# Performance work log

Hardware: AMD Instinct MI355X
Metric: run time of the kernel (lower is better)

Reference implementation:

```python
import jax, jax.numpy as jnp
import numpy as np

EPS = 1e-6
NEG = -1e9
RES_RATIO = 1.0  # res_ratio init arg
MAKE_SYM = True


def _ln(x, g, b):
    m = jnp.mean(x, axis=-1, keepdims=True)
    v = jnp.mean((x - m) ** 2, axis=-1, keepdims=True)
    return (x - m) * jax.lax.rsqrt(v + EPS) * g + b


def _sim(q, k, W1q, W1k, b1, W2, b2):
    # NN(concat([q,k])) with first dense split into query/key halves:
    # relu(q@W1q + k@W1k + b1) @ W2 + b2  -> avoids materializing the 2d concat.
    qa = q @ W1q  # [b,n,sq,h]
    kb = k @ W1k  # [b,n,sk,h]
    h1 = jax.nn.relu(qa[:, :, :, None, :] + kb[:, :, None, :, :] + b1)  # [b,n,sq,sk,h]
    s = jnp.einsum('bnqkh,h->bnqk', h1, W2[:, 0]) + b2[0]
    if MAKE_SYM:
        qb = q @ W1k
        ka = k @ W1q
        h2 = jax.nn.relu(ka[:, :, None, :, :] + qb[:, :, :, None, :] + b1)
        s = s + jnp.einsum('bnqkh,h->bnqk', h2, W2[:, 0]) + b2[0]
    return s


def _attention(v, k, q, mask, Ww, bw, Wd, bd, W1q, W1k, b1, W2, b2):
    q = q @ Ww + bw
    k = k @ Ww + bw
    v = v @ Ww + bw
    logits = _sim(q, k, W1q, W1k, b1, W2, b2)
    if mask is not None:
        logits = logits + mask * NEG
    attn = jax.nn.softmax(logits, axis=-1)
    out = jnp.einsum('bnqk,bnkd->bnqd', attn, v)
    return out @ Wd + bd, attn


def setup_inputs() -> dict:
    key = jax.random.key(0)
    B, N, S, D, DFF, H = 4, 1, 256, 128, 512, 128
    ks = jax.random.split(key, 16)
    s = 0.02
    inp = {
        'x': jax.random.normal(ks[0], (B, N, S, D), jnp.float32),
        'enc_output': jax.random.normal(ks[1], (B, N, S, D), jnp.float32),
        'com_mask': jnp.zeros((B, N, S, S), jnp.float32),
        'dec_mask': jnp.zeros((B, N, S, S), jnp.float32),
        # shared pairwise-score MLP NN: Dense(H, relu) -> Dense(1)
        'W1q': jax.random.normal(ks[2], (D, H), jnp.float32) * s,
        'W1k': jax.random.normal(ks[3], (D, H), jnp.float32) * s,
        'b1': jnp.zeros((H,), jnp.float32),
        'W2': jax.random.normal(ks[4], (H, 1), jnp.float32) * s,
        'b2': jnp.zeros((1,), jnp.float32),
        # mha1 projections
        'Ww1': jax.random.normal(ks[5], (D, D), jnp.float32) * s,
        'bw1': jnp.zeros((D,), jnp.float32),
        'Wd1': jax.random.normal(ks[6], (D, D), jnp.float32) * s,
        'bd1': jnp.zeros((D,), jnp.float32),
        # mha2 projections
        'Ww2': jax.random.normal(ks[7], (D, D), jnp.float32) * s,
        'bw2': jnp.zeros((D,), jnp.float32),
        'Wd2': jax.random.normal(ks[8], (D, D), jnp.float32) * s,
        'bd2': jnp.zeros((D,), jnp.float32),
        # ffn
        'Wf1': jax.random.normal(ks[9], (D, DFF), jnp.float32) * s,
        'bf1': jnp.zeros((DFF,), jnp.float32),
        'Wf2': jax.random.normal(ks[10], (DFF, D), jnp.float32) * s,
        'bf2': jnp.zeros((D,), jnp.float32),
        # layernorms
        'ln1_g': jnp.ones((D,), jnp.float32), 'ln1_b': jnp.zeros((D,), jnp.float32),
        'ln2_g': jnp.ones((D,), jnp.float32), 'ln2_b': jnp.zeros((D,), jnp.float32),
        'ln3_g': jnp.ones((D,), jnp.float32), 'ln3_b': jnp.zeros((D,), jnp.float32),
    }
    return inp


def reference(x, enc_output, com_mask, dec_mask,
              W1q, W1k, b1, W2, b2,
              Ww1, bw1, Wd1, bd1,
              Ww2, bw2, Wd2, bd2,
              Wf1, bf1, Wf2, bf2,
              ln1_g, ln1_b, ln2_g, ln2_b, ln3_g, ln3_b):
    r = RES_RATIO
    # self-attention block (dropout inactive, eval mode)
    attn1, aw1 = _attention(x, x, x, com_mask, Ww1, bw1, Wd1, bd1, W1q, W1k, b1, W2, b2)
    out1 = _ln((2 - r) * attn1 + r * x, ln1_g, ln1_b)
    # cross-attention block
    attn2, aw2 = _attention(enc_output, enc_output, out1, dec_mask, Ww2, bw2, Wd2, bd2, W1q, W1k, b1, W2, b2)
    out2 = _ln((2 - r) * attn2 + r * out1, ln2_g, ln2_b)
    # ffn
    ffn = jax.nn.relu(out2 @ Wf1 + bf1) @ Wf2 + bf2
    out3 = _ln((2 - r) * ffn + r * out2, ln3_g, ln3_b)
    return out3
```

## Files before the change

### kernel.cpp

```cpp
#include <hip/hip_runtime.h>
#include <math.h>


#define LN_EPS 1e-6f
#define NEGV  (-1e9f)

constexpr int B = 4, S = 256, D = 128, H = 128, DFF = 512;
constexpr int R = B * S;
constexpr int LDW = H + 4;

struct P {
    const float *x, *enc, *com_mask, *dec_mask;
    const float *W1q, *W1k, *b1, *W2;
    const float *Ww1, *bw1, *Wd1, *bd1;
    const float *Ww2, *bw2, *Wd2, *bd2;
    const float *Wf1, *bf1, *Wf2, *bf2;
    const float *ln1g, *ln1b, *ln2g, *ln2b, *ln3g, *ln3b;
    float *out;
    float *xw, *qa, *kb, *kv2w, *kb2, *ka2, *qa2, *qb2;
    float *sbuf, *sbuf2, *out1;
};

__global__ __launch_bounds__(512) void proj3_kernel(P p)
{
    const int g = blockIdx.y, tid = threadIdx.x;
    const int r0 = blockIdx.x * 8;
    __shared__ __align__(16) float Ash[8 * 128];
    __shared__ __align__(16) float Pw[8 * 128];
    __shared__ __align__(16) float Pp[2 * 8 * 128];

    const float* A    = g ? p.enc  : p.x;
    const float* Wp   = g ? p.Ww2  : p.Ww1;
    const float* bp   = g ? p.bw2  : p.bw1;
    float*       o_w  = g ? p.kv2w : p.xw;
    const float* Wsec = g ? p.W1k  : p.W1q;
    const float* bsec = g ? nullptr: p.b1;
    float*       o_s  = g ? p.kb2  : p.qa;
    const float* Wthr = g ? p.W1q  : p.W1k;
    float*       o_t  = g ? p.ka2  : p.kb;

    if (tid < 256)
        ((float4*)Ash)[tid] = ((const float4*)(A + (size_t)r0 * 128))[tid];
    __syncthreads();

    {
        const int kh = tid >> 8, unit = tid & 255, lr = unit >> 5, c4 = unit & 31;
        const float4* W4 = (const float4*)Wp;
        float4 acc = (kh == 0) ? ((const float4*)bp)[c4] : make_float4(0.f, 0.f, 0.f, 0.f);
        const int k0 = kh * 64;
        #pragma unroll 8
        for (int k = 0; k < 64; ++k) {
            const float a = Ash[lr * 128 + k0 + k];
            const float4 w = W4[(k0 + k) * 32 + c4];
            acc.x = fmaf(a, w.x, acc.x); acc.y = fmaf(a, w.y, acc.y);
            acc.z = fmaf(a, w.z, acc.z); acc.w = fmaf(a, w.w, acc.w);
        }
        ((float4*)Pp)[kh * 256 + unit] = acc;
    }
    __syncthreads();
    if (tid < 256) {
        const int lr = tid >> 5, c4 = tid & 31;
        const float4 a = ((const float4*)Pp)[tid];
        const float4 bq = ((const float4*)Pp)[256 + tid];
        const float4 w = make_float4(a.x + bq.x, a.y + bq.y, a.z + bq.z, a.w + bq.w);
        ((float4*)Pw)[tid] = w;
        ((float4*)o_w)[(size_t)(r0 + lr) * 32 + c4] = w;
    }
    __syncthreads();

    {
        const int which = tid >> 8, unit = tid & 255, lr = unit >> 5, c4 = unit & 31;
        const float* W = which ? Wthr : Wsec;
        const float* bb = which ? nullptr : bsec;
        float* o = which ? o_t : o_s;
        const float4* W4 = (const float4*)W;
        float4 acc = bb ? ((const float4*)bb)[c4] : make_float4(0.f, 0.f, 0.f, 0.f);
        #pragma unroll 8
        for (int k = 0; k < 128; ++k) {
            const float a = Pw[lr * 128 + k];
            const float4 w = W4[k * 32 + c4];
            acc.x = fmaf(a, w.x, acc.x); acc.y = fmaf(a, w.y, acc.y);
            acc.z = fmaf(a, w.z, acc.z); acc.w = fmaf(a, w.w, acc.w);
        }
        ((float4*)o)[(size_t)(r0 + lr) * 32 + c4] = acc;
    }
}

#define PW_STEP_N(AP0, AP1, BP0, BP1, A00, A01, A10, A11)                      \
    {                                                                          \
        const float4 w  = *(const float4*)(W2s + h);                           \
        const float4 a0 = *(const float4*)((AP0) + h);                         \
        const float4 a1 = *(const float4*)((AP1) + h);                         \
        const float4 b0 = *(const float4*)((BP0) + h);                         \
        const float4 b1 = *(const float4*)((BP1) + h);                         \
        A00 = fmaf(fmaxf(a0.x+b0.x,0.f),w.x,A00); A00 = fmaf(fmaxf(a0.y+b0.y,0.f),w.y,A00); \
        A00 = fmaf(fmaxf(a0.z+b0.z,0.f),w.z,A00); A00 = fmaf(fmaxf(a0.w+b0.w,0.f),w.w,A00); \
        A01 = fmaf(fmaxf(a0.x+b1.x,0.f),w.x,A01); A01 = fmaf(fmaxf(a0.y+b1.y,0.f),w.y,A01); \
        A01 = fmaf(fmaxf(a0.z+b1.z,0.f),w.z,A01); A01 = fmaf(fmaxf(a0.w+b1.w,0.f),w.w,A01); \
        A10 = fmaf(fmaxf(a1.x+b0.x,0.f),w.x,A10); A10 = fmaf(fmaxf(a1.y+b0.y,0.f),w.y,A10); \
        A10 = fmaf(fmaxf(a1.z+b0.z,0.f),w.z,A10); A10 = fmaf(fmaxf(a1.w+b0.w,0.f),w.w,A10); \
        A11 = fmaf(fmaxf(a1.x+b1.x,0.f),w.x,A11); A11 = fmaf(fmaxf(a1.y+b1.y,0.f),w.y,A11); \
        A11 = fmaf(fmaxf(a1.z+b1.z,0.f),w.z,A11); A11 = fmaf(fmaxf(a1.w+b1.w,0.f),w.w,A11); \
    }

__global__ __launch_bounds__(512) void pairwise_self_kernel(P p)
{
    __shared__ __align__(16) float As[32 * LDW];
    __shared__ __align__(16) float Bs[32 * LDW];
    __shared__ __align__(16) float W2s[H];
    __shared__ __align__(16) float Pp[256 * 4];
    const int b = blockIdx.z, q0 = blockIdx.y * 32, k0 = blockIdx.x * 32;
    const int tid = threadIdx.x, bS = b * S;
    for (int i = tid; i < 32 * (H / 4); i += 512) {
        const int r = i >> 5, c4 = i & 31;
        ((float4*)(As + r * LDW))[c4] = ((const float4*)(p.qa + (size_t)(bS + q0 + r) * H))[c4];
        ((float4*)(Bs + r * LDW))[c4] = ((const float4*)(p.kb + (size_t)(bS + k0 + r) * H))[c4];
    }
    if (tid < H / 4) ((float4*)W2s)[tid] = ((const float4*)p.W2)[tid];
    __syncthreads();
    const int hh = tid >> 8, unit = tid & 255;
    const int tx = unit & 15, ty = unit >> 4;
    const float* A0 = As + (2 * ty) * LDW; const float* A1 = A0 + LDW;
    const float* B0 = Bs + (2 * tx) * LDW; const float* B1 = B0 + LDW;
    float acc00 = 0.f, acc01 = 0.f, acc10 = 0.f, acc11 = 0.f;
    const int hbase = hh * 64;
    #pragma unroll 4
    for (int hi = 0; hi < 64; hi += 4) {
        const int h = hbase + hi;
        PW_STEP_N(A0, A1, B0, B1, acc00, acc01, acc10, acc11);
    }
    if (hh) ((float4*)Pp)[unit] = make_float4(acc00, acc01, acc10, acc11);
    __syncthreads();
    if (!hh) {
        const float4 o = ((const float4*)Pp)[unit];
        const size_t base = (size_t)(bS + q0 + 2 * ty) * S + (k0 + 2 * tx);
        *(float2*)(p.sbuf + base)     = make_float2(acc00 + o.x, acc01 + o.y);
        *(float2*)(p.sbuf + base + S) = make_float2(acc10 + o.z, acc11 + o.w);
    }
}

__global__ __launch_bounds__(512) void pairwise_cross2_kernel(P p)
{
    __shared__ __align__(16) float As1[32 * LDW];
    __shared__ __align__(16) float Bs1[32 * LDW];
    __shared__ __align__(16) float As2[32 * LDW];
    __shared__ __align__(16) float Bs2[32 * LDW];
    __shared__ __align__(16) float W2s[H];
    __shared__ __align__(16) float Pp8[256 * 8];
    const int b = blockIdx.z, q0 = blockIdx.y * 32, k0 = blockIdx.x * 32;
    const int tid = threadIdx.x, bS = b * S;

    for (int i = tid; i < 32 * (H / 4); i += 512) {
        const int r = i >> 5, c4 = i & 31;
        ((float4*)(As1 + r * LDW))[c4] = ((const float4*)(p.qa2 + (size_t)(bS + q0 + r) * H))[c4];
        ((float4*)(Bs1 + r * LDW))[c4] = ((const float4*)(p.kb2 + (size_t)(bS + k0 + r) * H))[c4];
        ((float4*)(As2 + r * LDW))[c4] = ((const float4*)(p.qb2 + (size_t)(bS + q0 + r) * H))[c4];
        ((float4*)(Bs2 + r * LDW))[c4] = ((const float4*)(p.ka2 + (size_t)(bS + k0 + r) * H))[c4];
    }
    if (tid < H / 4) ((float4*)W2s)[tid] = ((const float4*)p.W2)[tid];
    __syncthreads();

    const int hh = tid >> 8, unit = tid & 255;
    const int tx = unit & 15, ty = unit >> 4;
    const float* A0 = As1 + (2 * ty) * LDW; const float* A1 = A0 + LDW;
    const float* B0 = Bs1 + (2 * tx) * LDW; const float* B1 = B0 + LDW;
    const float* C0 = As2 + (2 * ty) * LDW; const float* C1 = C0 + LDW;
    const float* D0 = Bs2 + (2 * tx) * LDW; const float* D1 = D0 + LDW;
    float a00 = 0.f, a01 = 0.f, a10 = 0.f, a11 = 0.f;
    float b00 = 0.f, b01 = 0.f, b10 = 0.f, b11 = 0.f;
    const int hbase = hh * 64;
    #pragma unroll 4
    for (int hi = 0; hi < 64; hi += 4) {
        const int h = hbase + hi;
        PW_STEP_N(A0, A1, B0, B1, a00, a01, a10, a11);
        PW_STEP_N(C0, C1, D0, D1, b00, b01, b10, b11);
    }
    if (hh) {
        ((float4*)Pp8)[unit * 2]     = make_float4(a00, a01, a10, a11);
        ((float4*)Pp8)[unit * 2 + 1] = make_float4(b00, b01, b10, b11);
    }
    __syncthreads();
    if (!hh) {
        const float4 o1 = ((const float4*)Pp8)[unit * 2];
        const float4 o2 = ((const float4*)Pp8)[unit * 2 + 1];
        const size_t base = (size_t)(bS + q0 + 2 * ty) * S + (k0 + 2 * tx);
        *(float2*)(p.sbuf2 + base)     = make_float2(a00 + b00 + o1.x + o2.x, a01 + b01 + o1.y + o2.y);
        *(float2*)(p.sbuf2 + base + S) = make_float2(a10 + b10 + o1.z + o2.z, a11 + b11 + o1.w + o2.w);
    }
}

template<bool SYM, bool QPROJ, bool FFN>
__global__ __launch_bounds__(512) void attn_tail_kernel(P p)
{
    __shared__ __align__(16) float smem[FFN ? 16896 : 6144];
    float* rowS = smem;
    float* s8   = smem + 512;
    float* avp  = smem + 1536;
    float* aoS  = smem + 3584;
    float* pp   = smem + 4096;

    const float* Sin  = SYM ? p.sbuf : p.sbuf2;
    const float* mask = SYM ? p.com_mask : p.dec_mask;
    const float* V    = SYM ? p.xw : p.kv2w;
    const float* Wd   = SYM ? p.Wd1 : p.Wd2;
    const float* bd   = SYM ? p.bd1 : p.bd2;
    const float* res  = SYM ? p.x : p.out1;
    const float* lg   = SYM ? p.ln1g : p.ln2g;
    const float* lb   = SYM ? p.ln1b : p.ln2b;

    const int tid = threadIdx.x;
    const int r0 = blockIdx.x * 4, b = r0 >> 8, bS = b * S;

    for (int i = tid; i < 4 * 256; i += 512) {
        const int r = i >> 8, k = i & 255;
        const int row = r0 + r, q = row & 255;
        float l = Sin[(size_t)row * S + k];
        if (SYM) l += Sin[(size_t)(bS + k) * S + q];
        l += mask[(size_t)row * S + k] * NEGV;
        s8[i] = l;
    }
    __syncthreads();

    {
        const int g = tid >> 6, c = tid & 63;
        if (g < 4) {
            float* rowp = s8 + g * 256;
            float m = -INFINITY;
            #pragma unroll
            for (int k = c; k < 256; k += 64) m = fmaxf(m, rowp[k]);
            for (int o = 32; o; o >>= 1) m = fmaxf(m, __shfl_xor(m, o, 64));
            float s = 0.f;
            #pragma unroll
            for (int k = c; k < 256; k += 64) { const float e = __expf(rowp[k] - m); rowp[k] = e; s += e; }
            for (int o = 32; o; o >>= 1) s += __shfl_xor(s, o, 64);
            const float rinv = 1.f / s;
            #pragma unroll
            for (int k = c; k < 256; k += 64) rowp[k] *= rinv;
        }
    }
    __syncthreads();

    {
        const int r = tid >> 7, t = tid & 127, kq = t >> 5, c4 = t & 31;
        const float4* V4 = (const float4*)(V + (size_t)bS * D);
        const float* sp = s8 + r * 256 + kq * 64;
        float4 acc = make_float4(0.f, 0.f, 0.f, 0.f);
        #pragma unroll 8
        for (int k = 0; k < 64; ++k) {
            const float a = sp[k];
            const float4 v = V4[(kq * 64 + k) * 32 + c4];
            acc.x = fmaf(a, v.x, acc.x); acc.y = fmaf(a, v.y, acc.y);
            acc.z = fmaf(a, v.z, acc.z); acc.w = fmaf(a, v.w, acc.w);
        }
        ((float4*)avp)[(r * 4 + kq) * 32 + c4] = acc;
    }
    __syncthreads();
    if (tid < 128) {
        const int r = tid >> 5, c4 = tid & 31;
        float4 s0 = ((const float4*)avp)[(r * 4 + 0) * 32 + c4];
        const float4 s1 = ((const float4*)avp)[(r * 4 + 1) * 32 + c4];
        const float4 s2 = ((const float4*)avp)[(r * 4 + 2) * 32 + c4];
        const float4 s3 = ((const float4*)avp)[(r * 4 + 3) * 32 + c4];
        s0.x += s1.x + s2.x + s3.x; s0.y += s1.y + s2.y + s3.y;
        s0.z += s1.z + s2.z + s3.z; s0.w += s1.w + s2.w + s3.w;
        ((float4*)aoS)[r * 32 + c4] = s0;
    }
    __syncthreads();

    {
        const int kq = tid >> 7, unit = tid & 127, r = unit >> 5, c4 = unit & 31;
        const float4* W4 = (const float4*)Wd;
        const float* ap = aoS + r * 128 + kq * 32;
        float4 acc = make_float4(0.f, 0.f, 0.f, 0.f);
        #pragma unroll 8
        for (int k = 0; k < 32; ++k) {
            const float a = ap[k];
            const float4 w = W4[(kq * 32 + k) * 32 + c4];
            acc.x = fmaf(a, w.x, acc.x); acc.y = fmaf(a, w.y, acc.y);
            acc.z = fmaf(a, w.z, acc.z); acc.w = fmaf(a, w.w, acc.w);
        }
        ((float4*)pp)[kq * 128 + unit] = acc;
    }
    __syncthreads();

    if (tid < 128) {
        const int r = tid >> 5, c4 = tid & 31;
        const float4 p0 = ((const float4*)pp)[tid];
        const float4 p1 = ((const float4*)pp)[128 + tid];
        const float4 p2 = ((const float4*)pp)[256 + tid];
        const float4 p3 = ((const float4*)pp)[384 + tid];
        const float4 bv0 = ((const float4*)bd)[c4];
        const float4 r4 = ((const float4*)(res + (size_t)(r0 + r) * 128))[c4];
        const float x0 = p0.x + p1.x + p2.x + p3.x + bv0.x + r4.x;
        const float x1 = p0.y + p1.y + p2.y + p3.y + bv0.y + r4.y;
        const float x2 = p0.z + p1.z + p2.z + p3.z + bv0.z + r4.z;
        const float x3 = p0.w + p1.w + p2.w + p3.w + bv0.w + r4.w;
        float s  = x0 + x1 + x2 + x3;
        float s2 = x0 * x0 + x1 * x1 + x2 * x2 + x3 * x3;
        for (int o = 16; o; o >>= 1) { s += __shfl_xor(s, o, 32); s2 += __shfl_xor(s2, o, 32); }
        const float m = s * (1.f / 128), var = s2 * (1.f / 128) - m * m;
        const float rs = rsqrtf(var + LN_EPS);
        const float4 gv = ((const float4*)lg)[c4], bv = ((const float4*)lb)[c4];
        float4 o4;
        o4.x = (x0 - m) * rs * gv.x + bv.x; o4.y = (x1 - m) * rs * gv.y + bv.y;
        o4.z = (x2 - m) * rs * gv.z + bv.z; o4.w = (x3 - m) * rs * gv.w + bv.w;
        ((float4*)rowS)[r * 32 + c4] = o4;
        if (SYM) ((float4*)p.out1)[(size_t)(r0 + r) * 32 + c4] = o4;
    }
    __syncthreads();

    if (QPROJ) {
        float* qpp  = smem + 512;
        float* q2wS = smem + 2560;
        float* qp2  = smem + 1536;
        {
            const int kq = tid >> 7, unit = tid & 127, r = unit >> 5, c4 = unit & 31;
            const float4* W4 = (const float4*)p.Ww2;
            const float* ap = rowS + r * 128 + kq * 32;
            float4 acc = make_float4(0.f, 0.f, 0.f, 0.f);
            #pragma unroll 8
            for (int k = 0; k < 32; ++k) {
                const float a = ap[k];
                const float4 w = W4[(kq * 32 + k) * 32 + c4];
                acc.x = fmaf(a, w.x, acc.x); acc.y = fmaf(a, w.y, acc.y);
                acc.z = fmaf(a, w.z, acc.z); acc.w = fmaf(a, w.w, acc.w);
            }
            ((float4*)qpp)[kq * 128 + unit] = acc;
        }
        __syncthreads();
        if (tid < 128) {
            const int c4 = tid & 31;
            const float4 p0 = ((const float4*)qpp)[tid];
            const float4 p1 = ((const float4*)qpp)[128 + tid];
            const float4 p2 = ((const float4*)qpp)[256 + tid];
            const float4 p3 = ((const float4*)qpp)[384 + tid];
            const float4 bw = ((const float4*)p.bw2)[c4];
            ((float4*)q2wS)[tid] = make_float4(p0.x + p1.x + p2.x + p3.x + bw.x,
                                               p0.y + p1.y + p2.y + p3.y + bw.y,
                                               p0.z + p1.z + p2.z + p3.z + bw.z,
                                               p0.w + p1.w + p2.w + p3.w + bw.w);
        }
        __syncthreads();
        {
            const int which = tid >> 8, sub = tid & 255;
            const int kh = sub >> 7, unit2 = sub & 127;
            const float4* W4 = (const float4*)(which ? p.W1k : p.W1q);
            const int r = unit2 >> 5, c4 = unit2 & 31;
            const float* ap = q2wS + r * 128 + kh * 64;
            float4 acc = make_float4(0.f, 0.f, 0.f, 0.f);
            #pragma unroll 8
            for (int k = 0; k < 64; ++k) {
                const float a = ap[k];
                const float4 w = W4[(kh * 64 + k) * 32 + c4];
                acc.x = fmaf(a, w.x, acc.x); acc.y = fmaf(a, w.y, acc.y);
                acc.z = fmaf(a, w.z, acc.z); acc.w = fmaf(a, w.w, acc.w);
            }
            ((float4*)qp2)[(which * 2 + kh) * 128 + unit2] = acc;
        }
        __syncthreads();
        if (tid < 256) {
            const int which = tid >> 7, unit2 = tid & 127;
            const int r = unit2 >> 5, c4 = unit2 & 31;
            const float4 p0 = ((const float4*)qp2)[(which * 2 + 0) * 128 + unit2];
            const float4 p1 = ((const float4*)qp2)[(which * 2 + 1) * 128 + unit2];
            const float4 b1v = ((const float4*)p.b1)[c4];
            float* oq = which ? p.qb2 : p.qa2;
            ((float4*)oq)[(size_t)(r0 + r) * 32 + c4] =
                make_float4(p0.x + p1.x + b1v.x, p0.y + p1.y + b1v.y,
                            p0.z + p1.z + b1v.z, p0.w + p1.w + b1v.w);
        }
    }

    if (FFN) {
        float* hidP = smem + 512;
        float* part = smem + 8704;
        {
            const int c = tid & 127, kh = tid >> 7;
            const float4* Wf1_4 = (const float4*)p.Wf1;
            float4 a0 = make_float4(0.f,0.f,0.f,0.f), a1 = a0, a2 = a0, a3 = a0;
            const int kbase = kh * 32;
            #pragma unroll 8
            for (int k = 0; k < 32; ++k) {
                const int kk = kbase + k;
                const float4 w = Wf1_4[kk * 128 + c];
                const float s0 = rowS[kk],       s1 = rowS[128 + kk];
                const float s2 = rowS[256 + kk], s3 = rowS[384 + kk];
                a0.x=fmaf(s0,w.x,a0.x); a0.y=fmaf(s0,w.y,a0.y); a0.z=fmaf(s0,w.z,a0.z); a0.w=fmaf(s0,w.w,a0.w);
                a1.x=fmaf(s1,w.x,a1.x); a1.y=fmaf(s1,w.y,a1.y); a1.z=fmaf(s1,w.z,a1.z); a1.w=fmaf(s1,w.w,a1.w);
                a2.x=fmaf(s2,w.x,a2.x); a2.y=fmaf(s2,w.y,a2.y); a2.z=fmaf(s2,w.z,a2.z); a2.w=fmaf(s2,w.w,a2.w);
                a3.x=fmaf(s3,w.x,a3.x); a3.y=fmaf(s3,w.y,a3.y); a3.z=fmaf(s3,w.z,a3.z); a3.w=fmaf(s3,w.w,a3.w);
            }
            float4* h4 = (float4*)hidP;
            const int base = kh * 512;
            h4[base + 0*128 + c] = a0; h4[base + 1*128 + c] = a1;
            h4[base + 2*128 + c] = a2; h4[base + 3*128 + c] = a3;
        }
        __syncthreads();
        for (int i = tid; i < 2048; i += 512) {
            hidP[i] = fmaxf(hidP[i] + hidP[2048 + i] + hidP[4096 + i] + hidP[6144 + i]
                            + p.bf1[i & 511], 0.f);
        }
        __syncthreads();
        {
            const int c4f = tid & 31, kg = tid >> 5;
            const float4* Wf2_4 = (const float4*)p.Wf2;
            float4 a0 = make_float4(0.f,0.f,0.f,0.f), a1 = a0, a2 = a0, a3 = a0;
            const int kbase = kg * 32;
            const float* h0 = hidP + 0 * 512 + kbase;
            const float* h1 = hidP + 1 * 512 + kbase;
            const float* h2 = hidP + 2 * 512 + kbase;
            const float* h3 = hidP + 3 * 512 + kbase;
            #pragma unroll 8
            for (int k = 0; k < 32; ++k) {
                const float4 w = Wf2_4[(kbase + k) * 32 + c4f];
                const float s0 = h0[k], s1 = h1[k], s2 = h2[k], s3 = h3[k];
                a0.x=fmaf(s0,w.x,a0.x); a0.y=fmaf(s0,w.y,a0.y); a0.z=fmaf(s0,w.z,a0.z); a0.w=fmaf(s0,w.w,a0.w);
                a1.x=fmaf(s1,w.x,a1.x); a1.y=fmaf(s1,w.y,a1.y); a1.z=fmaf(s1,w.z,a1.z); a1.w=fmaf(s1,w.w,a1.w);
                a2.x=fmaf(s2,w.x,a2.x); a2.y=fmaf(s2,w.y,a2.y); a2.z=fmaf(s2,w.z,a2.z); a2.w=fmaf(s2,w.w,a2.w);
                a3.x=fmaf(s3,w.x,a3.x); a3.y=fmaf(s3,w.y,a3.y); a3.z=fmaf(s3,w.z,a3.z); a3.w=fmaf(s3,w.w,a3.w);
            }
            float4* p4 = (float4*)part;
            p4[kg * 128 + 0 * 32 + c4f] = a0; p4[kg * 128 + 1 * 32 + c4f] = a1;
            p4[kg * 128 + 2 * 32 + c4f] = a2; p4[kg * 128 + 3 * 32 + c4f] = a3;
        }
        __syncthreads();
        if (tid < 128) {
            const int r = tid >> 5, c4 = tid & 31;
            const float4* p4 = (const float4*)part;
            float4 sum = ((const float4*)p.bf2)[c4];
            #pragma unroll
            for (int kg = 0; kg < 16; ++kg) {
                const float4 v = p4[kg * 128 + r * 32 + c4];
                sum.x += v.x; sum.y += v.y; sum.z += v.z; sum.w += v.w;
            }
            const float4 r4 = ((const float4*)rowS)[r * 32 + c4];
            const float x0 = sum.x + r4.x, x1 = sum.y + r4.y;
            const float x2 = sum.z + r4.z, x3 = sum.w + r4.w;
            float s  = x0 + x1 + x2 + x3;
            float s2 = x0 * x0 + x1 * x1 + x2 * x2 + x3 * x3;
            for (int o = 16; o; o >>= 1) { s += __shfl_xor(s, o, 32); s2 += __shfl_xor(s2, o, 32); }
            const float m = s * (1.f / 128), var = s2 * (1.f / 128) - m * m;
            const float rs = rsqrtf(var + LN_EPS);
            const float4 gv = ((const float4*)p.ln3g)[c4], bv = ((const float4*)p.ln3b)[c4];
            float4 o4;
            o4.x = (x0 - m) * rs * gv.x + bv.x; o4.y = (x1 - m) * rs * gv.y + bv.y;
            o4.z = (x2 - m) * rs * gv.z + bv.z; o4.w = (x3 - m) * rs * gv.w + bv.w;
            ((float4*)p.out)[(size_t)(r0 + r) * 32 + c4] = o4;
        }
    }
}

extern "C" void kernel_launch(void* const* d_in, const int* in_sizes, int n_in,
                              void* d_out, int out_size, void* d_ws, size_t ws_size,
                              hipStream_t stream) {
    (void)in_sizes; (void)n_in; (void)out_size; (void)ws_size;
    P p;
    p.x        = (const float*)d_in[0];
    p.enc      = (const float*)d_in[1];
    p.com_mask = (const float*)d_in[2];
    p.dec_mask = (const float*)d_in[3];
    p.W1q = (const float*)d_in[4];
    p.W1k = (const float*)d_in[5];
    p.b1  = (const float*)d_in[6];
    p.W2  = (const float*)d_in[7];
    p.Ww1 = (const float*)d_in[9];
    p.bw1 = (const float*)d_in[10];
    p.Wd1 = (const float*)d_in[11];
    p.bd1 = (const float*)d_in[12];
    p.Ww2 = (const float*)d_in[13];
    p.bw2 = (const float*)d_in[14];
    p.Wd2 = (const float*)d_in[15];
    p.bd2 = (const float*)d_in[16];
    p.Wf1 = (const float*)d_in[17];
    p.bf1 = (const float*)d_in[18];
    p.Wf2 = (const float*)d_in[19];
    p.bf2 = (const float*)d_in[20];
    p.ln1g = (const float*)d_in[21];
    p.ln1b = (const float*)d_in[22];
    p.ln2g = (const float*)d_in[23];
    p.ln2b = (const float*)d_in[24];
    p.ln3g = (const float*)d_in[25];
    p.ln3b = (const float*)d_in[26];
    p.out  = (float*)d_out;

    float* ws = (float*)d_ws;
    const size_t RD  = (size_t)R * D;
    const size_t SSz = (size_t)B * S * S;
    p.xw    = ws;
    p.qa    = p.xw    + RD;
    p.kb    = p.qa    + RD;
    p.kv2w  = p.kb    + RD;
    p.kb2   = p.kv2w  + RD;
    p.ka2   = p.kb2   + RD;
    p.qa2   = p.ka2   + RD;
    p.qb2   = p.qa2   + RD;
    p.sbuf  = p.qb2   + RD;
    p.sbuf2 = p.sbuf  + SSz;
    p.out1  = p.sbuf2 + SSz;

    proj3_kernel<<<dim3(R / 8, 2), 512, 0, stream>>>(p);
    pairwise_self_kernel<<<dim3(8, 8, 4), 512, 0, stream>>>(p);
    attn_tail_kernel<true, true, false><<<R / 4, 512, 0, stream>>>(p);
    pairwise_cross2_kernel<<<dim3(8, 8, 4), 512, 0, stream>>>(p);
    attn_tail_kernel<false, false, true><<<R / 4, 512, 0, stream>>>(p);
}
```

Before: 172.0 us.

## Fuse pairwise score MLP into attention tail kernels, drop score buffers

Folds the pairwise relu-MLP score computation into each attention tail block. Each block of 4 query rows streams all 256 keys through shared memory in 64-key tiles and reduces across 8 lanes with shuffles. Symmetrization is done directly with both terms for the self block, so the S×S score buffers and two kernel launches go away. The trade-off is that each of the 256 blocks recomputes over all keys with only 4 query rows of reuse, which adds key-side global and LDS traffic per block.

```diff
diff --git a/kernel.cpp b/kernel.cpp
--- a/kernel.cpp
+++ b/kernel.cpp
@@ -7,7 +7,7 @@
 
 constexpr int B = 4, S = 256, D = 128, H = 128, DFF = 512;
 constexpr int R = B * S;
-constexpr int LDW = H + 4;
+constexpr int SP = 132;
 
 struct P {
     const float *x, *enc, *com_mask, *dec_mask;
@@ -17,8 +17,7 @@
     const float *Wf1, *bf1, *Wf2, *bf2;
     const float *ln1g, *ln1b, *ln2g, *ln2b, *ln3g, *ln3b;
     float *out;
-    float *xw, *qa, *kb, *kv2w, *kb2, *ka2, *qa2, *qb2;
-    float *sbuf, *sbuf2, *out1;
+    float *xw, *qa, *kb, *kv2w, *kb2, *ka2, *qa2, *qb2, *out1;
 };
 
 __global__ __launch_bounds__(512) void proj3_kernel(P p)
@@ -86,138 +85,105 @@
     }
 }
 
-#define PW_STEP_N(AP0, AP1, BP0, BP1, A00, A01, A10, A11)                      \
-    {                                                                          \
-        const float4 w  = *(const float4*)(W2s + h);                           \
-        const float4 a0 = *(const float4*)((AP0) + h);                         \
-        const float4 a1 = *(const float4*)((AP1) + h);                         \
-        const float4 b0 = *(const float4*)((BP0) + h);                         \
-        const float4 b1 = *(const float4*)((BP1) + h);                         \
-        A00 = fmaf(fmaxf(a0.x+b0.x,0.f),w.x,A00); A00 = fmaf(fmaxf(a0.y+b0.y,0.f),w.y,A00); \
-        A00 = fmaf(fmaxf(a0.z+b0.z,0.f),w.z,A00); A00 = fmaf(fmaxf(a0.w+b0.w,0.f),w.w,A00); \
-        A01 = fmaf(fmaxf(a0.x+b1.x,0.f),w.x,A01); A01 = fmaf(fmaxf(a0.y+b1.y,0.f),w.y,A01); \
-        A01 = fmaf(fmaxf(a0.z+b1.z,0.f),w.z,A01); A01 = fmaf(fmaxf(a0.w+b1.w,0.f),w.w,A01); \
-        A10 = fmaf(fmaxf(a1.x+b0.x,0.f),w.x,A10); A10 = fmaf(fmaxf(a1.y+b0.y,0.f),w.y,A10); \
-        A10 = fmaf(fmaxf(a1.z+b0.z,0.f),w.z,A10); A10 = fmaf(fmaxf(a1.w+b0.w,0.f),w.w,A10); \
-        A11 = fmaf(fmaxf(a1.x+b1.x,0.f),w.x,A11); A11 = fmaf(fmaxf(a1.y+b1.y,0.f),w.y,A11); \
-        A11 = fmaf(fmaxf(a1.z+b1.z,0.f),w.z,A11); A11 = fmaf(fmaxf(a1.w+b1.w,0.f),w.w,A11); \
-    }
-
-__global__ __launch_bounds__(512) void pairwise_self_kernel(P p)
+#define SC8(ACC, O1, X1, O2, X2)                                               \
+    ACC = fmaf(fmaxf((O1).x + (X1).x, 0.f), w.x, ACC);                         \
+    ACC = fmaf(fmaxf((O1).y + (X1).y, 0.f), w.y, ACC);                         \
+    ACC = fmaf(fmaxf((O1).z + (X1).z, 0.f), w.z, ACC);                         \
+    ACC = fmaf(fmaxf((O1).w + (X1).w, 0.f), w.w, ACC);                         \
+    ACC = fmaf(fmaxf((O2).x + (X2).x, 0.f), w.x, ACC);                         \
+    ACC = fmaf(fmaxf((O2).y + (X2).y, 0.f), w.y, ACC);                         \
+    ACC = fmaf(fmaxf((O2).z + (X2).z, 0.f), w.z, ACC);                         \
+    ACC = fmaf(fmaxf((O2).w + (X2).w, 0.f), w.w, ACC);
+
+template<bool FIRST>
+__global__ __launch_bounds__(512) void fused_attn_kernel(P p)
 {
-    __shared__ __align__(16) float As[32 * LDW];
-    __shared__ __align__(16) float Bs[32 * LDW];
-    __shared__ __align__(16) float W2s[H];
-    __shared__ __align__(16) float Pp[256 * 4];
-    const int b = blockIdx.z, q0 = blockIdx.y * 32, k0 = blockIdx.x * 32;
-    const int tid = threadIdx.x, bS = b * S;
-    for (int i = tid; i < 32 * (H / 4); i += 512) {
-        const int r = i >> 5, c4 = i & 31;
-        ((float4*)(As + r * LDW))[c4] = ((const float4*)(p.qa + (size_t)(bS + q0 + r) * H))[c4];
-        ((float4*)(Bs + r * LDW))[c4] = ((const float4*)(p.kb + (size_t)(bS + k0 + r) * H))[c4];
-    }
-    if (tid < H / 4) ((float4*)W2s)[tid] = ((const float4*)p.W2)[tid];
-    __syncthreads();
-    const int hh = tid >> 8, unit = tid & 255;
-    const int tx = unit & 15, ty = unit >> 4;
-    const float* A0 = As + (2 * ty) * LDW; const float* A1 = A0 + LDW;
-    const float* B0 = Bs + (2 * tx) * LDW; const float* B1 = B0 + LDW;
-    float acc00 = 0.f, acc01 = 0.f, acc10 = 0.f, acc11 = 0.f;
-    const int hbase = hh * 64;
-    #pragma unroll 4
-    for (int hi = 0; hi < 64; hi += 4) {
-        const int h = hbase + hi;
-        PW_STEP_N(A0, A1, B0, B1, acc00, acc01, acc10, acc11);
-    }
-    if (hh) ((float4*)Pp)[unit] = make_float4(acc00, acc01, acc10, acc11);
-    __syncthreads();
-    if (!hh) {
-        const float4 o = ((const float4*)Pp)[unit];
-        const size_t base = (size_t)(bS + q0 + 2 * ty) * S + (k0 + 2 * tx);
-        *(float2*)(p.sbuf + base)     = make_float2(acc00 + o.x, acc01 + o.y);
-        *(float2*)(p.sbuf + base + S) = make_float2(acc10 + o.z, acc11 + o.w);
-    }
-}
-
-__global__ __launch_bounds__(512) void pairwise_cross2_kernel(P p)
-{
-    __shared__ __align__(16) float As1[32 * LDW];
-    __shared__ __align__(16) float Bs1[32 * LDW];
-    __shared__ __align__(16) float As2[32 * LDW];
-    __shared__ __align__(16) float Bs2[32 * LDW];
-    __shared__ __align__(16) float W2s[H];
-    __shared__ __align__(16) float Pp8[256 * 8];
-    const int b = blockIdx.z, q0 = blockIdx.y * 32, k0 = blockIdx.x * 32;
-    const int tid = threadIdx.x, bS = b * S;
-
-    for (int i = tid; i < 32 * (H / 4); i += 512) {
-        const int r = i >> 5, c4 = i & 31;
-        ((float4*)(As1 + r * LDW))[c4] = ((const float4*)(p.qa2 + (size_t)(bS + q0 + r) * H))[c4];
-        ((float4*)(Bs1 + r * LDW))[c4] = ((const float4*)(p.kb2 + (size_t)(bS + k0 + r) * H))[c4];
-        ((float4*)(As2 + r * LDW))[c4] = ((const float4*)(p.qb2 + (size_t)(bS + q0 + r) * H))[c4];
-        ((float4*)(Bs2 + r * LDW))[c4] = ((const float4*)(p.ka2 + (size_t)(bS + k0 + r) * H))[c4];
-    }
-    if (tid < H / 4) ((float4*)W2s)[tid] = ((const float4*)p.W2)[tid];
-    __syncthreads();
-
-    const int hh = tid >> 8, unit = tid & 255;
-    const int tx = unit & 15, ty = unit >> 4;
-    const float* A0 = As1 + (2 * ty) * LDW; const float* A1 = A0 + LDW;
-    const float* B0 = Bs1 + (2 * tx) * LDW; const float* B1 = B0 + LDW;
-    const float* C0 = As2 + (2 * ty) * LDW; const float* C1 = C0 + LDW;
-    const float* D0 = Bs2 + (2 * tx) * LDW; const float* D1 = D0 + LDW;
-    float a00 = 0.f, a01 = 0.f, a10 = 0.f, a11 = 0.f;
-    float b00 = 0.f, b01 = 0.f, b10 = 0.f, b11 = 0.f;
-    const int hbase = hh * 64;
-    #pragma unroll 4
-    for (int hi = 0; hi < 64; hi += 4) {
-        const int h = hbase + hi;
-        PW_STEP_N(A0, A1, B0, B1, a00, a01, a10, a11);
-        PW_STEP_N(C0, C1, D0, D1, b00, b01, b10, b11);
-    }
-    if (hh) {
-        ((float4*)Pp8)[unit * 2]     = make_float4(a00, a01, a10, a11);
-        ((float4*)Pp8)[unit * 2 + 1] = make_float4(b00, b01, b10, b11);
-    }
-    __syncthreads();
-    if (!hh) {
-        const float4 o1 = ((const float4*)Pp8)[unit * 2];
-        const float4 o2 = ((const float4*)Pp8)[unit * 2 + 1];
-        const size_t base = (size_t)(bS + q0 + 2 * ty) * S + (k0 + 2 * tx);
-        *(float2*)(p.sbuf2 + base)     = make_float2(a00 + b00 + o1.x + o2.x, a01 + b01 + o1.y + o2.y);
-        *(float2*)(p.sbuf2 + base + S) = make_float2(a10 + b10 + o1.z + o2.z, a11 + b11 + o1.w + o2.w);
-    }
-}
-
-template<bool SYM, bool QPROJ, bool FFN>
-__global__ __launch_bounds__(512) void attn_tail_kernel(P p)
-{
-    __shared__ __align__(16) float smem[FFN ? 16896 : 6144];
-    float* rowS = smem;
-    float* s8   = smem + 512;
-    float* avp  = smem + 1536;
-    float* aoS  = smem + 3584;
-    float* pp   = smem + 4096;
-
-    const float* Sin  = SYM ? p.sbuf : p.sbuf2;
-    const float* mask = SYM ? p.com_mask : p.dec_mask;
-    const float* V    = SYM ? p.xw : p.kv2w;
-    const float* Wd   = SYM ? p.Wd1 : p.Wd2;
-    const float* bd   = SYM ? p.bd1 : p.bd2;
-    const float* res  = SYM ? p.x : p.out1;
-    const float* lg   = SYM ? p.ln1g : p.ln2g;
-    const float* lb   = SYM ? p.ln1b : p.ln2b;
+    __shared__ __align__(16) float smem[18432];
+    float* s8   = smem;
+    float* rowS = smem + 1024;
 
     const int tid = threadIdx.x;
     const int r0 = blockIdx.x * 4, b = r0 >> 8, bS = b * S;
 
-    for (int i = tid; i < 4 * 256; i += 512) {
+    const float* O1g  = FIRST ? p.qa  : p.qa2;
+    const float* O2g  = FIRST ? p.kb  : p.qb2;
+    const float* S1g  = FIRST ? p.kb  : p.kb2;
+    const float* S2g  = FIRST ? p.qa  : p.ka2;
+    const float* mask = FIRST ? p.com_mask : p.dec_mask;
+    const float* V    = FIRST ? p.xw : p.kv2w;
+    const float* Wd   = FIRST ? p.Wd1 : p.Wd2;
+    const float* bd   = FIRST ? p.bd1 : p.bd2;
+    const float* res  = FIRST ? p.x : p.out1;
+    const float* lg   = FIRST ? p.ln1g : p.ln2g;
+    const float* lb   = FIRST ? p.ln1b : p.ln2b;
+
+    {
+        float* stg1 = smem + 1536;
+        float* stg2 = smem + 9984;
+        const int hh = tid & 7, unit = tid >> 3, kk = unit & 31, rg = unit >> 5;
+        const int rA = r0 + 2 * rg, rB = rA + 1;
+
+        float4 o1A[4], o1B[4], o2A[4], o2B[4], w2r[4];
+        #pragma unroll
+        for (int j = 0; j < 4; ++j) {
+            const int h = hh * 4 + 32 * j;
+            o1A[j] = *(const float4*)(O1g + (size_t)rA * H + h);
+            o1B[j] = *(const float4*)(O1g + (size_t)rB * H + h);
+            o2A[j] = *(const float4*)(O2g + (size_t)rA * H + h);
+            o2B[j] = *(const float4*)(O2g + (size_t)rB * H + h);
+            w2r[j] = *(const float4*)(p.W2 + h);
+        }
+
+        for (int kt = 0; kt < 4; ++kt) {
+            #pragma unroll
+            for (int t = 0; t < 8; ++t) {
+                const int fi = tid + t * 512;
+                const int arr = fi >> 11, row = (fi >> 5) & 63, cf = (fi & 31) * 4;
+                const float* gp = (arr ? S2g : S1g) + (size_t)(bS + kt * 64 + row) * H + cf;
+                float* dp = (arr ? stg2 : stg1) + row * SP + cf;
+                *(float4*)dp = *(const float4*)gp;
+            }
+            __syncthreads();
+
+            const float* s1a = stg1 + kk * SP;
+            const float* s1b = stg1 + (kk + 32) * SP;
+            const float* s2a = stg2 + kk * SP;
+            const float* s2b = stg2 + (kk + 32) * SP;
+            float aAa = 0.f, aAb = 0.f, aBa = 0.f, aBb = 0.f;
+            #pragma unroll
+            for (int j = 0; j < 4; ++j) {
+                const int h = hh * 4 + 32 * j;
+                const float4 w = w2r[j];
+                const float4 x1a = *(const float4*)(s1a + h);
+                const float4 x1b = *(const float4*)(s1b + h);
+                const float4 x2a = *(const float4*)(s2a + h);
+                const float4 x2b = *(const float4*)(s2b + h);
+                SC8(aAa, o1A[j], x1a, o2A[j], x2a)
+                SC8(aAb, o1A[j], x1b, o2A[j], x2b)
+                SC8(aBa, o1B[j], x1a, o2B[j], x2a)
+                SC8(aBb, o1B[j], x1b, o2B[j], x2b)
+            }
+            #pragma unroll
+            for (int o = 1; o < 8; o <<= 1) {
+                aAa += __shfl_xor(aAa, o, 8);
+                aAb += __shfl_xor(aAb, o, 8);
+                aBa += __shfl_xor(aBa, o, 8);
+                aBb += __shfl_xor(aBb, o, 8);
+            }
+            if (hh == 0) {
+                const int kb0 = kt * 64;
+                s8[(2 * rg)     * 256 + kb0 + kk]      = aAa;
+                s8[(2 * rg)     * 256 + kb0 + kk + 32] = aAb;
+                s8[(2 * rg + 1) * 256 + kb0 + kk]      = aBa;
+                s8[(2 * rg + 1) * 256 + kb0 + kk + 32] = aBb;
+            }
+            __syncthreads();
+        }
+    }
+
+    for (int i = tid; i < 1024; i += 512) {
         const int r = i >> 8, k = i & 255;
-        const int row = r0 + r, q = row & 255;
-        float l = Sin[(size_t)row * S + k];
-        if (SYM) l += Sin[(size_t)(bS + k) * S + q];
-        l += mask[(size_t)row * S + k] * NEGV;
-        s8[i] = l;
+        s8[i] += mask[(size_t)(r0 + r) * S + k] * NEGV;
     }
     __syncthreads();
 
@@ -239,6 +205,10 @@
         }
     }
     __syncthreads();
+
+    float* avp = smem + 1536;
+    float* aoS = smem + 3584;
+    float* pp  = smem + 4096;
 
     {
         const int r = tid >> 7, t = tid & 127, kq = t >> 5, c4 = t & 31;
@@ -305,14 +275,14 @@
         o4.x = (x0 - m) * rs * gv.x + bv.x; o4.y = (x1 - m) * rs * gv.y + bv.y;
         o4.z = (x2 - m) * rs * gv.z + bv.z; o4.w = (x3 - m) * rs * gv.w + bv.w;
         ((float4*)rowS)[r * 32 + c4] = o4;
-        if (SYM) ((float4*)p.out1)[(size_t)(r0 + r) * 32 + c4] = o4;
-    }
-    __syncthreads();
-
-    if (QPROJ) {
-        float* qpp  = smem + 512;
-        float* q2wS = smem + 2560;
-        float* qp2  = smem + 1536;
+        if (FIRST) ((float4*)p.out1)[(size_t)(r0 + r) * 32 + c4] = o4;
+    }
+    __syncthreads();
+
+    if (FIRST) {
+        float* qpp  = smem + 6144;
+        float* q2wS = smem + 8192;
+        float* qp2  = smem + 8704;
         {
             const int kq = tid >> 7, unit = tid & 127, r = unit >> 5, c4 = unit & 31;
             const float4* W4 = (const float4*)p.Ww2;
@@ -369,11 +339,9 @@
                 make_float4(p0.x + p1.x + b1v.x, p0.y + p1.y + b1v.y,
                             p0.z + p1.z + b1v.z, p0.w + p1.w + b1v.w);
         }
-    }
-
-    if (FFN) {
-        float* hidP = smem + 512;
-        float* part = smem + 8704;
+    } else {
+        float* hidP = smem + 1536;
+        float* part = smem + 9984;
         {
             const int c = tid & 127, kh = tid >> 7;
             const float4* Wf1_4 = (const float4*)p.Wf1;
@@ -484,8 +452,7 @@
     p.out  = (float*)d_out;
 
     float* ws = (float*)d_ws;
-    const size_t RD  = (size_t)R * D;
-    const size_t SSz = (size_t)B * S * S;
+    const size_t RD = (size_t)R * D;
     p.xw    = ws;
     p.qa    = p.xw    + RD;
     p.kb    = p.qa    + RD;
@@ -494,13 +461,9 @@
     p.ka2   = p.kb2   + RD;
     p.qa2   = p.ka2   + RD;
     p.qb2   = p.qa2   + RD;
-    p.sbuf  = p.qb2   + RD;
-    p.sbuf2 = p.sbuf  + SSz;
-    p.out1  = p.sbuf2 + SSz;
+    p.out1  = p.qb2   + RD;
 
     proj3_kernel<<<dim3(R / 8, 2), 512, 0, stream>>>(p);
-    pairwise_self_kernel<<<dim3(8, 8, 4), 512, 0, stream>>>(p);
-    attn_tail_kernel<true, true, false><<<R / 4, 512, 0, stream>>>(p);
-    pairwise_cross2_kernel<<<dim3(8, 8, 4), 512, 0, stream>>>(p);
-    attn_tail_kernel<false, false, true><<<R / 4, 512, 0, stream>>>(p);
+    fused_attn_kernel<true><<<R / 4, 512, 0, stream>>>(p);
+    fused_attn_kernel<false><<<R / 4, 512, 0, stream>>>(p);
 }
```

Result: no change. 174.1 us (+1.2%).
